# Optimization experiments

Measured on AMD Instinct MI355X. Metric: run time of the kernel, lower is better.

## Reference

```python
import jax, jax.numpy as jnp
import numpy as np

D_MODEL = 512
N_HEADS = 8
NUM_NODES = 20
EPS = 1e-5

def _layer_norm(x, g, b):
    mu = jnp.mean(x, axis=-1, keepdims=True)
    var = jnp.var(x, axis=-1, keepdims=True)
    return (x - mu) * jax.lax.rsqrt(var + EPS) * g + b

def _conv1d(x_bcn, w_oik):
    # x: [B, C, N], w: [O, I, K], padding = K//2 (same)
    k = w_oik.shape[-1]
    p = k // 2
    return jax.lax.conv_general_dilated(
        x_bcn, w_oik, window_strides=(1,), padding=[(p, p)],
        dimension_numbers=('NCH', 'OIH', 'NCH'))

def setup_inputs() -> dict:
    key = jax.random.key(0)
    ks = jax.random.split(key, 6)
    B, N, D, H = 4096, NUM_NODES, D_MODEL, N_HEADS
    x = jax.random.normal(ks[0], (B, N, D), dtype=jnp.float32)
    s = 1.0 / np.sqrt(D * 3)
    Wq = jax.random.normal(ks[1], (D, D, 3), dtype=jnp.float32) * s
    Wk = jax.random.normal(ks[2], (D, D, 3), dtype=jnp.float32) * s
    Wv = jax.random.normal(ks[3], (D, D, 3), dtype=jnp.float32) * s
    rel_table = jax.random.normal(ks[4], (2 * N - 1, H), dtype=jnp.float32) * 0.02
    Wo = jax.random.normal(ks[5], (D, D), dtype=jnp.float32) * (1.0 / np.sqrt(D))
    bo = jnp.zeros((D,), dtype=jnp.float32)
    ones = jnp.ones((D,), dtype=jnp.float32)
    zeros = jnp.zeros((D,), dtype=jnp.float32)
    return {"x": x, "Wq": Wq, "Wk": Wk, "Wv": Wv,
            "lnq_g": ones, "lnq_b": zeros, "lnk_g": ones, "lnk_b": zeros,
            "lnv_g": ones, "lnv_b": zeros,
            "rel_table": rel_table, "Wo": Wo, "bo": bo}

def reference(x, Wq, Wk, Wv, lnq_g, lnq_b, lnk_g, lnk_b, lnv_g, lnv_b, rel_table, Wo, bo):
    B, N, D = x.shape
    H = N_HEADS
    dk = D // H
    x_p = jnp.transpose(x, (0, 2, 1))  # [B, D, N]

    def proj(W, g, b):
        c = _conv1d(x_p, W)                      # [B, D, N]
        c = _layer_norm(jnp.transpose(c, (0, 2, 1)), g, b)  # [B, N, D]
        return x + c                              # residual

    q = proj(Wq, lnq_g, lnq_b)
    k = proj(Wk, lnk_g, lnk_b)
    v = proj(Wv, lnv_g, lnv_b)

    q = q.reshape(B, N, H, dk).transpose(0, 2, 1, 3)  # [B,H,N,dk]
    k = k.reshape(B, N, H, dk).transpose(0, 2, 1, 3)
    v = v.reshape(B, N, H, dk).transpose(0, 2, 1, 3)

    scale = 1.0 / np.sqrt(dk)
    scores = jnp.einsum('bhnd,bhmd->bhnm', q, k) * scale  # [B,H,N,N]

    # relative position bias: index[i,j] = i - j + N - 1
    coords = jnp.arange(N)
    rel_idx = coords[:, None] - coords[None, :] + (N - 1)   # [N,N]
    rel_bias = rel_table[rel_idx]                            # [N,N,H]
    rel_bias = jnp.transpose(rel_bias, (2, 0, 1))[None]      # [1,H,N,N]
    scores = scores + rel_bias

    attn = jax.nn.softmax(scores, axis=-1)
    out = jnp.einsum('bhnm,bhmd->bhnd', attn, v)             # [B,H,N,dk]
    out = out.transpose(0, 2, 1, 3).reshape(B, N, D)
    return out @ Wo.T + bo
```

## Files before the change

kernel.cpp:

```cpp
#include <hip/hip_runtime.h>
#include <hip/hip_bf16.h>
#include <stdint.h>

typedef __attribute__((ext_vector_type(8))) __bf16 bf16x8;
typedef __attribute__((ext_vector_type(4))) float f32x4;

#define B_TOT   4096
#define NN      20
#define DM      512
#define NC1     1536
#define M_TOT   (B_TOT*NN)
#define NPAD    22

__device__ __forceinline__ void async_copy16(const __bf16* g, __bf16* l) {
    __builtin_amdgcn_global_load_lds(
        (__attribute__((address_space(1))) void*)g,
        (__attribute__((address_space(3))) void*)l, 16, 0, 0);
}

template<typename T>
__device__ __forceinline__ void load8(const T* p, float* r) {
    if constexpr (sizeof(T) == 4) {
        f32x4 a = *(const f32x4*)p;
        f32x4 b = *(const f32x4*)(p + 4);
#pragma unroll
        for (int i = 0; i < 4; ++i) { r[i] = a[i]; r[i + 4] = b[i]; }
    } else {
        bf16x8 a = *(const bf16x8*)p;
#pragma unroll
        for (int i = 0; i < 8; ++i) r[i] = (float)a[i];
    }
}

__global__ void detect_kernel(const uint32_t* __restrict__ xw, int* __restrict__ mode) {
    int lane = threadIdx.x & 63;
    int susp = 0;
#pragma unroll
    for (int i = 0; i < 4; ++i) {
        uint32_t w = xw[lane * 4 + i];
        uint32_t e = (w >> 7) & 0xFF;
        if ((e >= 118 && e <= 130) || (w & 0xFFFFu) == 0) susp++;
    }
#pragma unroll
    for (int o = 32; o > 0; o >>= 1) susp += __shfl_xor(susp, o, 64);
    if (lane == 0) *mode = (susp > 128) ? 1 : 0;
}

template<typename T>
__device__ __forceinline__ void wt_body(
    const T* __restrict__ Wq, const T* __restrict__ Wk, const T* __restrict__ Wv,
    const T* __restrict__ Wo, __bf16* __restrict__ Wt, __bf16* __restrict__ Wob, int f)
{
    if (f < 1536 * 1536) {
        int col = f / 1536, k = f - col * 1536;
        int p = col >> 9, o = col & 511;
        int kap = k >> 9, i = k & 511;
        const T* W = (p == 0) ? Wq : ((p == 1) ? Wk : Wv);
        Wt[f] = (__bf16)(float)W[(o * 512 + i) * 3 + kap];
    } else {
        int g = f - 1536 * 1536;
        Wob[g] = (__bf16)(float)Wo[g];
    }
}

__global__ __launch_bounds__(256) void wt_kernel(
    const void* Wq, const void* Wk, const void* Wv, const void* Wo,
    __bf16* Wt, __bf16* Wob, const int* mode)
{
    int f = blockIdx.x * 256 + threadIdx.x;
    if (*mode)
        wt_body<__bf16>((const __bf16*)Wq, (const __bf16*)Wk, (const __bf16*)Wv,
                        (const __bf16*)Wo, Wt, Wob, f);
    else
        wt_body<float>((const float*)Wq, (const float*)Wk, (const float*)Wv,
                       (const float*)Wo, Wt, Wob, f);
}

template<typename T>
__device__ __forceinline__ void xpad_body(
    const T* __restrict__ x, __bf16* __restrict__ xp, int idx)
{
    int col = (idx & 63) * 8;
    int row = idx >> 6;
    int b = row / 22;
    int np = row - b * 22;
    bf16x8 ov;
    if (np == 0 || np == 21) {
#pragma unroll
        for (int t = 0; t < 8; ++t) ov[t] = (__bf16)0.f;
    } else {
        float tmp[8];
        load8<T>(x + ((size_t)(b * 20 + np - 1) * 512 + col), tmp);
#pragma unroll
        for (int t = 0; t < 8; ++t) ov[t] = (__bf16)tmp[t];
    }
    *(bf16x8*)(xp + (size_t)row * 512 + col) = ov;
}

__global__ __launch_bounds__(256) void xpad_kernel(
    const void* x, __bf16* xp, const int* mode)
{
    int idx = blockIdx.x * 256 + threadIdx.x;
    if (*mode) xpad_body<__bf16>((const __bf16*)x, xp, idx);
    else       xpad_body<float>((const float*)x, xp, idx);
}

#define SBAR()  __builtin_amdgcn_s_barrier()
#define SCHED0() __builtin_amdgcn_sched_barrier(0)
#define LGKM0() do { asm volatile("s_waitcnt lgkmcnt(0)" ::: "memory"); SCHED0(); } while (0)
#define VM4()   do { SCHED0(); asm volatile("s_waitcnt vmcnt(4)" ::: "memory"); } while (0)
#define VM0()   do { SCHED0(); asm volatile("s_waitcnt vmcnt(0)" ::: "memory"); } while (0)

__device__ __forceinline__ void g1_loadA(const __bf16* slab, int off, bf16x8 (&aq)[4]) {
#pragma unroll
    for (int i = 0; i < 4; ++i) aq[i] = *(const bf16x8*)(slab + off + i * 512);
}
__device__ __forceinline__ void g1_loadB(const __bf16* slab, int off, bf16x8 (&bq)[4]) {
#pragma unroll
    for (int i = 0; i < 4; ++i) bq[i] = *(const bf16x8*)(slab + off + i * 512);
}
template<int QM>
__device__ __forceinline__ void g1_mma(bf16x8 (&aq)[4], bf16x8 (&bq)[4], f32x4 (&acc)[8][4]) {
    __builtin_amdgcn_s_setprio(1);
#pragma unroll
    for (int i = 0; i < 4; ++i)
#pragma unroll
        for (int nf = 0; nf < 4; ++nf)
            acc[QM * 4 + i][nf] = __builtin_amdgcn_mfma_f32_16x16x32_bf16(
                aq[i], bq[nf], acc[QM * 4 + i][nf], 0, 0, 0);
    __builtin_amdgcn_s_setprio(0);
}

__global__ __launch_bounds__(512, 2) void g1_kernel(
    const __bf16* __restrict__ xpad, const __bf16* __restrict__ Wt,
    __bf16* __restrict__ Cout, int mbase)
{
    extern __shared__ __align__(16) __bf16 sh[];
    __bf16* shA = sh;
    __bf16* shB = sh + 32768;

    const int tid = threadIdx.x;
    const int w = tid >> 6, l = tid & 63;
    const int lr = l & 15, lq = l >> 4;
    const int wm = w >> 2, wn = w & 3;

    int nwg = gridDim.x;
    int bid = blockIdx.x;
    if ((nwg & 7) == 0) bid = (bid & 7) * (nwg >> 3) + (bid >> 3);
    const int nb = bid % 6;
    const int mb = bid / 6;
    const int n0 = nb * 256;
    const int mloc = mb * 256;

    const int rin = l >> 2;
    const int pc  = (l & 3) * 8;
    const int lc  = (rin >= 8) ? (pc ^ 16) : pc;
    const int R0 = w * 16 + rin;
    const int R1 = 128 + R0;
    const int g0 = mbase + mloc + R0, g1r = mbase + mloc + R1;
    const __bf16* aP0 = xpad + (size_t)((g0 / 20) * 22 + g0 % 20) * 512 + lc;
    const __bf16* aP1 = xpad + (size_t)((g1r / 20) * 22 + g1r % 20) * 512 + lc;
    const __bf16* bP0 = Wt + (size_t)(n0 + R0) * 1536 + lc;
    const __bf16* bP1 = Wt + (size_t)(n0 + R1) * 1536 + lc;
    const int sdst = w * 512 + l * 8;

    const int swzcol = (lr >= 8) ? ((lq * 8) ^ 16) : (lq * 8);
    const int ardoff = lr * 32 + swzcol;
    const int rdA = wm * 8 * 512 + ardoff;
    const int rdB = wn * 4 * 512 + ardoff;

    f32x4 acc[8][4] = {};
    bf16x8 aq[4], bq[4];

    { __bf16* d = shA + 0 * 8192 + sdst; async_copy16(aP0 + 0, d);  async_copy16(aP1 + 0, d + 4096); }
    { __bf16* d = shB + 0 * 8192 + sdst; async_copy16(bP0 + 0, d);  async_copy16(bP1 + 0, d + 4096); }
    { __bf16* d = shA + 1 * 8192 + sdst; async_copy16(aP0 + 32, d); async_copy16(aP1 + 32, d + 4096); }
    { __bf16* d = shB + 1 * 8192 + sdst; async_copy16(bP0 + 32, d); async_copy16(bP1 + 32, d + 4096); }
    VM4();
    SBAR();

    for (int t = 0; t < 24; ++t) {
        const int cur = t & 1;
        const __bf16* A0 = shA + (cur * 2 + 0) * 8192;
        const __bf16* A1 = shA + (cur * 2 + 1) * 8192;
        const __bf16* B0 = shB + (cur * 2 + 0) * 8192;
        const __bf16* B1 = shB + (cur * 2 + 1) * 8192;
        __bf16* dA0 = shA + ((cur ^ 1) * 2 + 0) * 8192 + sdst;
        __bf16* dA1 = shA + ((cur ^ 1) * 2 + 1) * 8192 + sdst;
        __bf16* dB0 = shB + ((cur ^ 1) * 2 + 0) * 8192 + sdst;
        __bf16* dB1 = shB + ((cur ^ 1) * 2 + 1) * 8192 + sdst;
        const int kn = (t + 1) * 64;
        const bool st = (t < 23);

        g1_loadA(A0, rdA, aq);
        g1_loadB(B0, rdB, bq);
        if (st) { async_copy16(aP0 + kn, dA0); async_copy16(aP1 + kn, dA0 + 4096); }
        SBAR(); LGKM0();
        g1_mma<0>(aq, bq, acc);
        SBAR();

        g1_loadA(A0, rdA + 2048, aq);
        if (st) { async_copy16(bP0 + kn, dB0); async_copy16(bP1 + kn, dB0 + 4096); }
        if (st) VM4(); else VM0();
        SBAR(); LGKM0();
        g1_mma<1>(aq, bq, acc);
        SBAR();

        g1_loadA(A1, rdA, aq);
        g1_loadB(B1, rdB, bq);
        if (st) { async_copy16(aP0 + kn + 32, dA1); async_copy16(aP1 + kn + 32, dA1 + 4096); }
        SBAR(); LGKM0();
        g1_mma<0>(aq, bq, acc);
        SBAR();

        g1_loadA(A1, rdA + 2048, aq);
        if (st) { async_copy16(bP0 + kn + 32, dB1); async_copy16(bP1 + kn + 32, dB1 + 4096); }
        if (st) VM4();
        SBAR(); LGKM0();
        g1_mma<1>(aq, bq, acc);
        SBAR();
    }

#pragma unroll
    for (int mf = 0; mf < 8; ++mf) {
#pragma unroll
        for (int r = 0; r < 4; ++r) {
            int row = mloc + wm * 128 + mf * 16 + lq * 4 + r;
            size_t base = (size_t)row * 1536 + n0 + wn * 64 + lr;
#pragma unroll
            for (int nf = 0; nf < 4; ++nf)
                Cout[base + nf * 16] = (__bf16)acc[mf][nf][r];
        }
    }
}

template<typename T>
__device__ __forceinline__ void attn_body(
    const T* __restrict__ x, const __bf16* __restrict__ cqkv,
    const T* __restrict__ lnq_g, const T* __restrict__ lnq_b,
    const T* __restrict__ lnk_g, const T* __restrict__ lnk_b,
    const T* __restrict__ lnv_g, const T* __restrict__ lnv_b,
    const T* __restrict__ rel, __bf16* __restrict__ aout, int bbase,
    __bf16* sq , float* S , float* rb )
{
    const int tid = threadIdx.x;
    const int wave = tid >> 6, lane = tid & 63;
    const int bl = blockIdx.x;
    const size_t xbase = (size_t)(bbase + bl) * NN * DM;
    const size_t cbase = (size_t)bl * NN * NC1;

    for (int t = tid; t < 312; t += 256) rb[t] = (float)rel[t];

    for (int rr = 0; rr < 15; ++rr) {
        int row = wave * 15 + rr;
        int p = row / 20;
        int n = row - p * 20;
        bf16x8 cv = *(const bf16x8*)(cqkv + cbase + (size_t)n * NC1 + p * 512 + lane * 8);
        float vals[8]; float s = 0.f, ss = 0.f;
#pragma unroll
        for (int t = 0; t < 8; ++t) { float f = (float)cv[t]; vals[t] = f; s += f; ss += f * f; }
#pragma unroll
        for (int o = 32; o > 0; o >>= 1) { s += __shfl_xor(s, o, 64); ss += __shfl_xor(ss, o, 64); }
        float mu = s * (1.f / 512.f);
        float var = ss * (1.f / 512.f) - mu * mu;
        float rs = rsqrtf(var + 1e-5f);
        const T* g  = (p == 0) ? lnq_g : (p == 1) ? lnk_g : lnv_g;
        const T* bb = (p == 0) ? lnq_b : (p == 1) ? lnk_b : lnv_b;
        float gv[8], bv[8], xv[8];
        load8<T>(g  + lane * 8, gv);
        load8<T>(bb + lane * 8, bv);
        load8<T>(x + xbase + (size_t)n * DM + lane * 8, xv);
        bf16x8 ov;
#pragma unroll
        for (int t = 0; t < 8; ++t)
            ov[t] = (__bf16)((vals[t] - mu) * rs * gv[t] + bv[t] + xv[t]);
        *(bf16x8*)(sq + ((size_t)p * 20 + n) * 512 + lane * 8) = ov;
    }
    __syncthreads();

    if (tid < 160) {
        int h = tid / 20, j = tid - (tid / 20) * 20;
        float kreg[64];
        const __bf16* kr = sq + (size_t)(1 * 20 + j) * 512 + h * 64;
#pragma unroll
        for (int t = 0; t < 64; t += 8) {
            bf16x8 kv = *(const bf16x8*)(kr + t);
#pragma unroll
            for (int u = 0; u < 8; ++u) kreg[t + u] = (float)kv[u];
        }
        for (int i = 0; i < 20; ++i) {
            const __bf16* qr = sq + (size_t)(0 * 20 + i) * 512 + h * 64;
            float s = 0.f;
#pragma unroll
            for (int t = 0; t < 64; t += 8) {
                bf16x8 qv = *(const bf16x8*)(qr + t);
#pragma unroll
                for (int u = 0; u < 8; ++u) s += (float)qv[u] * kreg[t + u];
            }
            S[(h * 20 + i) * 20 + j] = s * 0.125f + rb[(i - j + 19) * 8 + h];
        }
    }
    __syncthreads();

    if (tid < 160) {
        int h = tid / 20, i = tid - (tid / 20) * 20;
        float* row = &S[(h * 20 + i) * 20];
        float mx = row[0];
        for (int j = 1; j < 20; ++j) mx = fmaxf(mx, row[j]);
        float e[20]; float sum = 0.f;
        for (int j = 0; j < 20; ++j) { e[j] = expf(row[j] - mx); sum += e[j]; }
        float inv = 1.f / sum;
        for (int j = 0; j < 20; ++j) row[j] = e[j] * inv;
    }
    __syncthreads();

    {
        int h = tid >> 5;
        int d2 = (tid & 31) * 2;
        float v0[20], v1[20];
#pragma unroll
        for (int j = 0; j < 20; ++j) {
            const __bf16* vr = sq + (size_t)(2 * 20 + j) * 512 + h * 64 + d2;
            v0[j] = (float)vr[0]; v1[j] = (float)vr[1];
        }
        for (int i = 0; i < 20; ++i) {
            float o0 = 0.f, o1 = 0.f;
#pragma unroll
            for (int j = 0; j < 20; ++j) {
                float p = S[(h * 20 + i) * 20 + j];
                o0 += p * v0[j]; o1 += p * v1[j];
            }
            __bf16* orow = aout + (size_t)(bl * NN + i) * DM + h * 64 + d2;
            orow[0] = (__bf16)o0;
            orow[1] = (__bf16)o1;
        }
    }
}

__global__ __launch_bounds__(256) void attn_kernel(
    const void* x, const __bf16* cqkv,
    const void* lnq_g, const void* lnq_b, const void* lnk_g, const void* lnk_b,
    const void* lnv_g, const void* lnv_b, const void* rel,
    __bf16* aout, int bbase, const int* mode)
{
    __shared__ __align__(16) __bf16 sq[3 * 20 * 512];
    __shared__ float S[8 * 20 * 20];
    __shared__ float rb[320];
    if (*mode)
        attn_body<__bf16>((const __bf16*)x, cqkv,
            (const __bf16*)lnq_g, (const __bf16*)lnq_b, (const __bf16*)lnk_g,
            (const __bf16*)lnk_b, (const __bf16*)lnv_g, (const __bf16*)lnv_b,
            (const __bf16*)rel, aout, bbase, sq, S, rb);
    else
        attn_body<float>((const float*)x, cqkv,
            (const float*)lnq_g, (const float*)lnq_b, (const float*)lnk_g,
            (const float*)lnk_b, (const float*)lnv_g, (const float*)lnv_b,
            (const float*)rel, aout, bbase, sq, S, rb);
}

template<typename T>
__device__ __forceinline__ void g3_body(
    const __bf16* __restrict__ Ain, const __bf16* __restrict__ Wob,
    const T* __restrict__ bo, T* __restrict__ out, int mbase,
    __bf16* As, __bf16* Bs)
{
    const int tid  = threadIdx.x;
    const int wave = tid >> 6, lane = tid & 63;
    const int n0 = blockIdx.x * 128;
    const int m0 = blockIdx.y * 128;
    const int srow = lane >> 3;
    const int scol = (lane & 7) * 8;
    const int lr = lane & 15, lq = lane >> 4;
    const int wm = (wave >> 1) * 64, wn = (wave & 1) * 64;
    f32x4 acc[4][4] = {};

    for (int kt = 0; kt < 8; ++kt) {
        const int k0 = kt * 64;
        __syncthreads();
#pragma unroll
        for (int j = 0; j < 4; ++j) {
            int rb_ = wave * 32 + j * 8;
            async_copy16(Ain + (size_t)(m0 + rb_ + srow) * 512 + (k0 + scol),
                         As + rb_ * 64 + lane * 8);
            async_copy16(Wob + (size_t)(n0 + rb_ + srow) * 512 + (k0 + scol),
                         Bs + rb_ * 64 + lane * 8);
        }
        __syncthreads();
#pragma unroll
        for (int ko = 0; ko < 64; ko += 32) {
            bf16x8 af[4], bfv[4];
#pragma unroll
            for (int mi = 0; mi < 4; ++mi)
                af[mi] = *(const bf16x8*)&As[(wm + mi * 16 + lr) * 64 + ko + lq * 8];
#pragma unroll
            for (int ni = 0; ni < 4; ++ni)
                bfv[ni] = *(const bf16x8*)&Bs[(wn + ni * 16 + lr) * 64 + ko + lq * 8];
#pragma unroll
            for (int mi = 0; mi < 4; ++mi)
#pragma unroll
                for (int ni = 0; ni < 4; ++ni)
                    acc[mi][ni] = __builtin_amdgcn_mfma_f32_16x16x32_bf16(
                        af[mi], bfv[ni], acc[mi][ni], 0, 0, 0);
        }
    }
#pragma unroll
    for (int mi = 0; mi < 4; ++mi) {
#pragma unroll
        for (int r = 0; r < 4; ++r) {
            int row = m0 + wm + mi * 16 + lq * 4 + r;
            size_t gbase = (size_t)(mbase + row) * 512 + n0 + wn + lr;
#pragma unroll
            for (int ni = 0; ni < 4; ++ni) {
                float bias = (float)bo[n0 + wn + lr + ni * 16];
                out[gbase + ni * 16] = (T)(acc[mi][ni][r] + bias);
            }
        }
    }
}

__global__ __launch_bounds__(256) void g3_kernel(
    const __bf16* Ain, const __bf16* Wob, const void* bo, void* out,
    int mbase, const int* mode)
{
    __shared__ __align__(16) __bf16 As[128 * 64];
    __shared__ __align__(16) __bf16 Bs[128 * 64];
    if (*mode) g3_body<__bf16>(Ain, Wob, (const __bf16*)bo, (__bf16*)out, mbase, As, Bs);
    else       g3_body<float>(Ain, Wob, (const float*)bo, (float*)out, mbase, As, Bs);
}

extern "C" void kernel_launch(void* const* d_in, const int* in_sizes, int n_in,
                              void* d_out, int out_size, void* d_ws, size_t ws_size,
                              hipStream_t stream) {
    (void)in_sizes; (void)n_in; (void)out_size;
    char* ws = (char*)d_ws;
    int*    mode = (int*)ws;
    __bf16* Wt   = (__bf16*)(ws + 256);
    __bf16* Wob  = (__bf16*)(ws + 256 + 4718592);
    __bf16* xpad = (__bf16*)(ws + 256 + 4718592 + 524288);
    const size_t off_c = 256 + 4718592 + 524288 + (size_t)B_TOT * NPAD * DM * 2;

    static bool attr_set = false;
    if (!attr_set) {
        (void)hipFuncSetAttribute((const void*)g1_kernel,
                                  hipFuncAttributeMaxDynamicSharedMemorySize, 131072);
        attr_set = true;
    }

    int CH = 1;
    while (CH < 64) {
        size_t rows = (size_t)M_TOT / CH;
        if (off_c + rows * (size_t)NC1 * 2 + rows * (size_t)DM * 2 <= ws_size) break;
        CH *= 2;
    }
    const int rows = M_TOT / CH;
    const int Bc   = B_TOT / CH;
    __bf16* Cbuf = (__bf16*)(ws + off_c);
    __bf16* Abuf = (__bf16*)(ws + off_c + (size_t)rows * NC1 * 2);

    detect_kernel<<<dim3(1), dim3(64), 0, stream>>>((const uint32_t*)d_in[0], mode);
    wt_kernel<<<dim3(10240), dim3(256), 0, stream>>>(
        d_in[1], d_in[2], d_in[3], d_in[11], Wt, Wob, mode);
    xpad_kernel<<<dim3(22528), dim3(256), 0, stream>>>(d_in[0], xpad, mode);

    for (int c = 0; c < CH; ++c) {
        int mbase = c * rows;
        g1_kernel<<<dim3(6 * (rows / 256)), dim3(512), 131072, stream>>>(
            xpad, Wt, Cbuf, mbase);
        attn_kernel<<<dim3(Bc), dim3(256), 0, stream>>>(
            d_in[0], Cbuf, d_in[4], d_in[5], d_in[6], d_in[7], d_in[8], d_in[9],
            d_in[10], Abuf, mbase / NN, mode);
        g3_kernel<<<dim3(4, rows / 128), dim3(256), 0, stream>>>(
            Abuf, Wob, d_in[12], d_out, mbase, mode);
    }
}
```

Measured before the change: 988.6 us.

## Restructure weight transpose, reuse padded bf16 x, stage attention output, chunk pipeline

Several independent changes. The weight transpose kernel now reads each conv weight triple once and writes three outputs, which cuts its thread count. The attention kernel reads the residual from the bf16 padded copy of x instead of the fp32 input, halving those reads. Attention outputs are staged in shared memory and written with coalesced 16-byte stores. The starting chunk count goes from 1 to 4 so the intermediate buffers stay smaller and more cache-resident, at the cost of extra kernel launches.

New measurement: 1.006 ms. About the same (+1.8%).

```diff
diff --git a/kernel.cpp b/kernel.cpp
--- a/kernel.cpp
+++ b/kernel.cpp
@@ -3,6 +3,7 @@
 #include <stdint.h>
 
 typedef __attribute__((ext_vector_type(8))) __bf16 bf16x8;
+typedef __attribute__((ext_vector_type(2))) __bf16 bf16x2;
 typedef __attribute__((ext_vector_type(4))) float f32x4;
 
 #define B_TOT   4096
@@ -49,17 +50,22 @@
 template<typename T>
 __device__ __forceinline__ void wt_body(
     const T* __restrict__ Wq, const T* __restrict__ Wk, const T* __restrict__ Wv,
-    const T* __restrict__ Wo, __bf16* __restrict__ Wt, __bf16* __restrict__ Wob, int f)
-{
-    if (f < 1536 * 1536) {
-        int col = f / 1536, k = f - col * 1536;
-        int p = col >> 9, o = col & 511;
-        int kap = k >> 9, i = k & 511;
+    const T* __restrict__ Wo, __bf16* __restrict__ Wt, __bf16* __restrict__ Wob, int t)
+{
+    if (t < 3 * 512 * 512) {
+        int p = t >> 18;
+        int r = t & 262143;
+        int o = r >> 9, i = r & 511;
         const T* W = (p == 0) ? Wq : ((p == 1) ? Wk : Wv);
-        Wt[f] = (__bf16)(float)W[(o * 512 + i) * 3 + kap];
+        const T* src = W + (size_t)(o * 512 + i) * 3;
+        float w0 = (float)src[0], w1 = (float)src[1], w2 = (float)src[2];
+        size_t base = (size_t)(p * 512 + o) * 1536 + i;
+        Wt[base]        = (__bf16)w0;
+        Wt[base + 512]  = (__bf16)w1;
+        Wt[base + 1024] = (__bf16)w2;
     } else {
-        int g = f - 1536 * 1536;
-        Wob[g] = (__bf16)(float)Wo[g];
+        int g2 = t - 3 * 512 * 512;
+        Wob[g2] = (__bf16)(float)Wo[g2];
     }
 }
 
@@ -67,13 +73,13 @@
     const void* Wq, const void* Wk, const void* Wv, const void* Wo,
     __bf16* Wt, __bf16* Wob, const int* mode)
 {
-    int f = blockIdx.x * 256 + threadIdx.x;
+    int t = blockIdx.x * 256 + threadIdx.x;
     if (*mode)
         wt_body<__bf16>((const __bf16*)Wq, (const __bf16*)Wk, (const __bf16*)Wv,
-                        (const __bf16*)Wo, Wt, Wob, f);
+                        (const __bf16*)Wo, Wt, Wob, t);
     else
         wt_body<float>((const float*)Wq, (const float*)Wk, (const float*)Wv,
-                       (const float*)Wo, Wt, Wob, f);
+                       (const float*)Wo, Wt, Wob, t);
 }
 
 template<typename T>
@@ -236,7 +242,7 @@
 
 template<typename T>
 __device__ __forceinline__ void attn_body(
-    const T* __restrict__ x, const __bf16* __restrict__ cqkv,
+    const __bf16* __restrict__ xpad, const __bf16* __restrict__ cqkv,
     const T* __restrict__ lnq_g, const T* __restrict__ lnq_b,
     const T* __restrict__ lnk_g, const T* __restrict__ lnk_b,
     const T* __restrict__ lnv_g, const T* __restrict__ lnv_b,
@@ -246,7 +252,7 @@
     const int tid = threadIdx.x;
     const int wave = tid >> 6, lane = tid & 63;
     const int bl = blockIdx.x;
-    const size_t xbase = (size_t)(bbase + bl) * NN * DM;
+    const size_t xpbase = ((size_t)(bbase + bl) * NPAD + 1) * DM;
     const size_t cbase = (size_t)bl * NN * NC1;
 
     for (int t = tid; t < 312; t += 256) rb[t] = (float)rel[t];
@@ -266,14 +272,14 @@
         float rs = rsqrtf(var + 1e-5f);
         const T* g  = (p == 0) ? lnq_g : (p == 1) ? lnk_g : lnv_g;
         const T* bb = (p == 0) ? lnq_b : (p == 1) ? lnk_b : lnv_b;
-        float gv[8], bv[8], xv[8];
+        float gv[8], bv[8];
         load8<T>(g  + lane * 8, gv);
         load8<T>(bb + lane * 8, bv);
-        load8<T>(x + xbase + (size_t)n * DM + lane * 8, xv);
+        bf16x8 xv = *(const bf16x8*)(xpad + xpbase + (size_t)n * DM + lane * 8);
         bf16x8 ov;
 #pragma unroll
         for (int t = 0; t < 8; ++t)
-            ov[t] = (__bf16)((vals[t] - mu) * rs * gv[t] + bv[t] + xv[t]);
+            ov[t] = (__bf16)((vals[t] - mu) * rs * gv[t] + bv[t] + (float)xv[t]);
         *(bf16x8*)(sq + ((size_t)p * 20 + n) * 512 + lane * 8) = ov;
     }
     __syncthreads();
@@ -330,15 +336,24 @@
                 float p = S[(h * 20 + i) * 20 + j];
                 o0 += p * v0[j]; o1 += p * v1[j];
             }
-            __bf16* orow = aout + (size_t)(bl * NN + i) * DM + h * 64 + d2;
-            orow[0] = (__bf16)o0;
-            orow[1] = (__bf16)o1;
+            bf16x2 pr; pr[0] = (__bf16)o0; pr[1] = (__bf16)o1;
+            *(bf16x2*)(sq + (size_t)i * 512 + h * 64 + d2) = pr;
+        }
+    }
+    __syncthreads();
+
+    {
+        __bf16* ab = aout + (size_t)bl * NN * DM;
+#pragma unroll
+        for (int e = 0; e < 5; ++e) {
+            int off = e * 2048 + tid * 8;
+            *(bf16x8*)(ab + off) = *(const bf16x8*)(sq + off);
         }
     }
 }
 
 __global__ __launch_bounds__(256) void attn_kernel(
-    const void* x, const __bf16* cqkv,
+    const __bf16* xpad, const __bf16* cqkv,
     const void* lnq_g, const void* lnq_b, const void* lnk_g, const void* lnk_b,
     const void* lnv_g, const void* lnv_b, const void* rel,
     __bf16* aout, int bbase, const int* mode)
@@ -347,12 +362,12 @@
     __shared__ float S[8 * 20 * 20];
     __shared__ float rb[320];
     if (*mode)
-        attn_body<__bf16>((const __bf16*)x, cqkv,
+        attn_body<__bf16>(xpad, cqkv,
             (const __bf16*)lnq_g, (const __bf16*)lnq_b, (const __bf16*)lnk_g,
             (const __bf16*)lnk_b, (const __bf16*)lnv_g, (const __bf16*)lnv_b,
             (const __bf16*)rel, aout, bbase, sq, S, rb);
     else
-        attn_body<float>((const float*)x, cqkv,
+        attn_body<float>(xpad, cqkv,
             (const float*)lnq_g, (const float*)lnq_b, (const float*)lnk_g,
             (const float*)lnk_b, (const float*)lnv_g, (const float*)lnv_b,
             (const float*)rel, aout, bbase, sq, S, rb);
@@ -446,7 +461,7 @@
         attr_set = true;
     }
 
-    int CH = 1;
+    int CH = 4;
     while (CH < 64) {
         size_t rows = (size_t)M_TOT / CH;
         if (off_c + rows * (size_t)NC1 * 2 + rows * (size_t)DM * 2 <= ws_size) break;
@@ -458,7 +473,7 @@
     __bf16* Abuf = (__bf16*)(ws + off_c + (size_t)rows * NC1 * 2);
 
     detect_kernel<<<dim3(1), dim3(64), 0, stream>>>((const uint32_t*)d_in[0], mode);
-    wt_kernel<<<dim3(10240), dim3(256), 0, stream>>>(
+    wt_kernel<<<dim3(4096), dim3(256), 0, stream>>>(
         d_in[1], d_in[2], d_in[3], d_in[11], Wt, Wob, mode);
     xpad_kernel<<<dim3(22528), dim3(256), 0, stream>>>(d_in[0], xpad, mode);
 
@@ -467,7 +482,7 @@
         g1_kernel<<<dim3(6 * (rows / 256)), dim3(512), 131072, stream>>>(
             xpad, Wt, Cbuf, mbase);
         attn_kernel<<<dim3(Bc), dim3(256), 0, stream>>>(
-            d_in[0], Cbuf, d_in[4], d_in[5], d_in[6], d_in[7], d_in[8], d_in[9],
+            xpad, Cbuf, d_in[4], d_in[5], d_in[6], d_in[7], d_in[8], d_in[9],
             d_in[10], Abuf, mbase / NN, mode);
         g3_kernel<<<dim3(4, rows / 128), dim3(256), 0, stream>>>(
             Abuf, Wob, d_in[12], d_out, mbase, mode);
```
